# Kernel optimization log

Measured on AMD Instinct MI355X. Metric: run time of the kernel, lower is better.

The kernel has to match this reference:

```python
import jax, jax.numpy as jnp
import numpy as np

EMBED_DIM = 1024
NUM_HEADS = 16
HEAD_DIM = EMBED_DIM // NUM_HEADS
B, T = 2, 2048


def setup_inputs() -> dict:
    key = jax.random.key(0)
    ks = jax.random.split(key, 5)
    s_in = 1.0 / np.sqrt(EMBED_DIM)
    return {
        "x": jax.random.normal(ks[0], (B, T, EMBED_DIM), dtype=jnp.float32),
        "qkv_w": jax.random.uniform(ks[1], (3 * EMBED_DIM, EMBED_DIM), jnp.float32, -s_in, s_in),
        "qkv_b": jax.random.uniform(ks[2], (3 * EMBED_DIM,), jnp.float32, -s_in, s_in),
        "out_w": jax.random.uniform(ks[3], (EMBED_DIM, EMBED_DIM), jnp.float32, -s_in, s_in),
        "out_b": jax.random.uniform(ks[4], (EMBED_DIM,), jnp.float32, -s_in, s_in),
    }


def reference(x, qkv_w, qkv_b, out_w, out_b):
    b, t, d = x.shape
    scale = HEAD_DIM ** -0.5
    # fused qkv projection: (B, T, 3D)
    qkv = jnp.einsum("btd,ed->bte", x, qkv_w) + qkv_b
    qkv = qkv.reshape(b, t, 3, NUM_HEADS, HEAD_DIM)
    q, k, v = jnp.moveaxis(qkv, 2, 0)  # each (B, T, H, Dh)
    # scores: (B, H, T, T)
    scores = jnp.einsum("bqhd,bkhd->bhqk", q, k) * scale
    attn = jax.nn.softmax(scores, axis=-1)
    # attention output: (B, T, H, Dh) -> (B, T, D)
    ctx = jnp.einsum("bhqk,bkhd->bqhd", attn, v).reshape(b, t, d)
    return jnp.einsum("btd,ed->bte", ctx, out_w) + out_b
```

## Files before the change

kernel.cpp:

```cpp
#include <hip/hip_runtime.h>

typedef __bf16 bf16;
typedef __bf16 bf16x4 __attribute__((ext_vector_type(4)));
typedef __bf16 bf16x8 __attribute__((ext_vector_type(8)));
typedef _Float16 f16;
typedef _Float16 f16x4 __attribute__((ext_vector_type(4)));
typedef _Float16 f16x8 __attribute__((ext_vector_type(8)));
typedef float f32x4 __attribute__((ext_vector_type(4)));
typedef unsigned int uint2t __attribute__((ext_vector_type(2)));
typedef unsigned int uint4t __attribute__((ext_vector_type(4)));

#define MFMA16(a, b, c) __builtin_amdgcn_mfma_f32_16x16x32_bf16(a, b, c, 0, 0, 0)
#define MFMA16F(a, b, c) __builtin_amdgcn_mfma_f32_16x16x32_f16(a, b, c, 0, 0, 0)

__device__ __forceinline__ void lds_load16(void* lds, const void* g) {
  __builtin_amdgcn_global_load_lds(
      (const __attribute__((address_space(1))) unsigned int*)g,
      (__attribute__((address_space(3))) unsigned int*)lds, 16, 0, 0);
}

__global__ void cvt3(const float* __restrict__ x, const float* __restrict__ qw,
                     const float* __restrict__ ow, bf16* __restrict__ xb,
                     bf16* __restrict__ qwb, f16* __restrict__ owb) {
  const int i = blockIdx.x * blockDim.x + threadIdx.x;
  if (i < 1048576 + 786432) {
    const float* src;
    bf16* dst;
    int k;
    if (i < 1048576) {
      src = x; dst = xb; k = i;
    } else {
      src = qw; dst = qwb; k = i - 1048576;
    }
    const float4 v = ((const float4*)src)[k];
    bf16x4 o;
    o[0] = (bf16)v.x; o[1] = (bf16)v.y; o[2] = (bf16)v.z; o[3] = (bf16)v.w;
    ((bf16x4*)dst)[k] = o;
  } else {
    const int k = i - (1048576 + 786432);
    const float4 v = ((const float4*)ow)[k];
    f16x4 o;
    o[0] = (f16)v.x; o[1] = (f16)v.y; o[2] = (f16)v.z; o[3] = (f16)v.w;
    ((f16x4*)owb)[k] = o;
  }
}

__global__ __launch_bounds__(256, 2) void gemm_qkv(
    const bf16* __restrict__ A, const bf16* __restrict__ B,
    const float* __restrict__ bias, bf16* __restrict__ Qb,
    bf16* __restrict__ KF, f16* __restrict__ VF) {
  const int K = 1024;
  __shared__ bf16 As[128][64];
  __shared__ bf16 Bs[128][64];
  const int tid = threadIdx.x;
  const int w = tid >> 6, lane = tid & 63;
  const int l15 = lane & 15, quad = lane >> 4;
  const int lr = lane >> 3;
  const int lcs = ((lane & 7) ^ lr) * 8;
  const int sw = l15 & 7;
  const int blk = blockIdx.x;
  const int xslot = blk & 7, rest = blk >> 3;
  const int bm = xslot * 4 + (rest & 3);
  const int bn = rest >> 2;
  const int wm = (w >> 1) * 64, wn = (w & 1) * 64;

  const bf16* Abase = A + (size_t)(bm * 128) * K;
  const bf16* Bbase = B + (size_t)(bn * 128) * K;

  f32x4 acc[4][4] = {};

  for (int k0 = 0; k0 < K; k0 += 64) {
#pragma unroll
    for (int c = 0; c < 4; ++c) {
      const int row = w * 32 + c * 8;
      lds_load16(&As[row][0], Abase + (size_t)(row + lr) * K + k0 + lcs);
      lds_load16(&Bs[row][0], Bbase + (size_t)(row + lr) * K + k0 + lcs);
    }
    __syncthreads();
#pragma unroll
    for (int kk = 0; kk < 64; kk += 32) {
      const int cb = kk >> 3;
      bf16x8 am[4], bnf[4];
#pragma unroll
      for (int i = 0; i < 4; ++i)
        am[i] = *(const bf16x8*)&As[wm + i * 16 + l15][((cb + quad) ^ sw) * 8];
#pragma unroll
      for (int j = 0; j < 4; ++j)
        bnf[j] = *(const bf16x8*)&Bs[wn + j * 16 + l15][((cb + quad) ^ sw) * 8];
#pragma unroll
      for (int i = 0; i < 4; ++i)
#pragma unroll
        for (int j = 0; j < 4; ++j)
          acc[i][j] = MFMA16(am[i], bnf[j], acc[i][j]);
    }
    __syncthreads();
  }

#pragma unroll
  for (int j = 0; j < 4; ++j) {
    const int gcol = bn * 128 + wn + j * 16 + l15;
    const float bv = bias[gcol];
#pragma unroll
    for (int i = 0; i < 4; ++i) {
      const int t0 = bm * 128 + wm + i * 16 + quad * 4;
      if (gcol < 1024) {
#pragma unroll
        for (int r = 0; r < 4; ++r)
          Qb[(size_t)(t0 + r) * 1024 + gcol] =
              (bf16)((acc[i][j][r] + bv) * 0.18033688f);
      } else if (gcol < 2048) {
        const int dhl = gcol - 1024;
        const int hh = dhl >> 6, dh = dhl & 63;
        const int tl = t0 & 2047, bb = t0 >> 11;
        const size_t frag = ((size_t)(bb * 16 + hh) * 32 + (tl >> 6)) * 8 +
                            ((tl & 63) >> 4) * 2 + (dh >> 5);
        bf16* p = &KF[frag * 512 +
                      (size_t)(((dh >> 3) & 3) * 16 + (tl & 15)) * 8 + (dh & 7)];
#pragma unroll
        for (int r = 0; r < 4; ++r) p[r * 8] = (bf16)(acc[i][j][r] + bv);
      } else {
        const int dhl = gcol - 2048;
        const int hh = dhl >> 6, dh = dhl & 63;
        const int tl = t0 & 2047, bb = t0 >> 11;
        const size_t frag = ((size_t)(bb * 16 + hh) * 32 + (tl >> 6)) * 8 +
                            (dh >> 4) * 2 + ((tl & 63) >> 5);
        f16x4 pv;
#pragma unroll
        for (int r = 0; r < 4; ++r) pv[r] = (f16)(acc[i][j][r] + bv);
        *(f16x4*)&VF[frag * 512 +
                     (size_t)(((tl & 31) >> 3) * 16 + (dh & 15)) * 8 +
                     (tl & 7)] = pv;
      }
    }
  }
}

__global__ __launch_bounds__(256, 2) void gemm_out(
    const f16* __restrict__ A, const f16* __restrict__ B,
    const float* __restrict__ bias, float* __restrict__ Cf) {
  __shared__ f16 As[64][64];
  __shared__ f16 Bs[128][64];
  const int tid = threadIdx.x;
  const int w = tid >> 6, lane = tid & 63;
  const int l15 = lane & 15, quad = lane >> 4;
  const int lr = lane >> 3;
  const int lcs = ((lane & 7) ^ lr) * 8;
  const int sw = l15 & 7;
  const int blk = blockIdx.x;
  const int xslot = blk & 7, rest = blk >> 3;
  const int bm = xslot * 8 + (rest & 7);
  const int bn = rest >> 3;

  const f16* Abase = A + (size_t)(bm * 64) * 1024;
  const f16* Bbase = B + (size_t)(bn * 128) * 1024;

  f32x4 acc[4][2] = {};

  for (int k0 = 0; k0 < 1024; k0 += 64) {
#pragma unroll
    for (int c = 0; c < 2; ++c) {
      const int row = w * 16 + c * 8;
      lds_load16(&As[row][0], Abase + (size_t)(row + lr) * 1024 + k0 + lcs);
    }
#pragma unroll
    for (int c = 0; c < 4; ++c) {
      const int row = w * 32 + c * 8;
      lds_load16(&Bs[row][0], Bbase + (size_t)(row + lr) * 1024 + k0 + lcs);
    }
    __syncthreads();
#pragma unroll
    for (int kk = 0; kk < 64; kk += 32) {
      const int cb = kk >> 3;
      f16x8 am[4], bnf[2];
#pragma unroll
      for (int i = 0; i < 4; ++i)
        am[i] = *(const f16x8*)&As[i * 16 + l15][((cb + quad) ^ sw) * 8];
#pragma unroll
      for (int j = 0; j < 2; ++j)
        bnf[j] =
            *(const f16x8*)&Bs[w * 32 + j * 16 + l15][((cb + quad) ^ sw) * 8];
#pragma unroll
      for (int i = 0; i < 4; ++i)
#pragma unroll
        for (int j = 0; j < 2; ++j)
          acc[i][j] = MFMA16F(am[i], bnf[j], acc[i][j]);
    }
    __syncthreads();
  }

#pragma unroll
  for (int j = 0; j < 2; ++j) {
    const int gcol = bn * 128 + w * 32 + j * 16 + l15;
    const float bv = bias[gcol];
#pragma unroll
    for (int i = 0; i < 4; ++i)
#pragma unroll
      for (int r = 0; r < 4; ++r) {
        const int grow = bm * 64 + i * 16 + quad * 4 + r;
        Cf[(size_t)grow * 1024 + gcol] = acc[i][j][r] + bv;
      }
  }
}

__global__ __launch_bounds__(512, 4) void attn(const bf16* __restrict__ Qb,
                                               const bf16* __restrict__ KF,
                                               const f16* __restrict__ VF,
                                               f16* __restrict__ CTX) {
  __shared__ bf16 KV[2][2][2][4096];
  const int tid = threadIdx.x, w = tid >> 6, lane = tid & 63;
  const int g = w >> 2, wg = w & 3;
  const int l15 = lane & 15, quad = lane >> 4;
  const int blk = blockIdx.x;
  const int slot = blk & 7, grp = blk >> 3;
  const int qt = grp & 15, bh = (grp >> 4) * 8 + slot;
  const int h = bh & 15, b = bh >> 4;
  const int q0 = qt * 128;

  const bf16* qrow0 =
      Qb + (size_t)(b * 2048 + q0 + wg * 32 + l15) * 1024 + h * 64;
  const bf16* qrow1 = qrow0 + (size_t)16 * 1024;
  const bf16x8 bq0a = *(const bf16x8*)&qrow0[quad * 8];
  const bf16x8 bq0b = *(const bf16x8*)&qrow0[32 + quad * 8];
  const bf16x8 bq1a = *(const bf16x8*)&qrow1[quad * 8];
  const bf16x8 bq1b = *(const bf16x8*)&qrow1[32 + quad * 8];

  const bf16* kfs = KF + (size_t)(b * 16 + h) * 131072 + (size_t)g * 65536;
  const f16* vfs = VF + (size_t)(b * 16 + h) * 131072 + (size_t)g * 65536;
  const int so = wg * 1024;

#pragma unroll
  for (int c = 0; c < 2; ++c) {
    lds_load16(&KV[g][0][0][so + c * 512], kfs + so + c * 512 + lane * 8);
    lds_load16(&KV[g][1][0][so + c * 512], vfs + so + c * 512 + lane * 8);
  }

  const f16x8 ones8 = {(f16)1, (f16)1, (f16)1, (f16)1,
                       (f16)1, (f16)1, (f16)1, (f16)1};
  f32x4 lsum[2] = {};
  f32x4 o[2][4] = {};

  for (int kt = 0; kt < 16; ++kt) {
    const int cur = kt & 1;
    const bf16* kcur = &KV[g][0][cur][0];
    const f16* vcur = (const f16*)&KV[g][1][cur][0];
    __syncthreads();

    if (kt < 15) {
      const size_t nb = (size_t)(kt + 1) * 4096;
#pragma unroll
      for (int c = 0; c < 2; ++c) {
        lds_load16(&KV[g][0][cur ^ 1][so + c * 512],
                   kfs + nb + so + c * 512 + lane * 8);
        lds_load16(&KV[g][1][cur ^ 1][so + c * 512],
                   vfs + nb + so + c * 512 + lane * 8);
      }
    }

    f32x4 s[2][4] = {};
#pragma unroll
    for (int k2 = 0; k2 < 2; ++k2)
#pragma unroll
      for (int j = 0; j < 4; ++j) {
        const bf16x8 ak = *(const bf16x8*)&kcur[(j * 2 + k2) * 512 + lane * 8];
        s[0][j] = MFMA16(ak, k2 ? bq0b : bq0a, s[0][j]);
        s[1][j] = MFMA16(ak, k2 ? bq1b : bq1a, s[1][j]);
      }

    f16x8 bp[2][2];
#pragma unroll
    for (int i = 0; i < 2; ++i) {
      uint2t pd[4];
#pragma unroll
      for (int j = 0; j < 4; ++j) {
        const auto lo =
            __builtin_amdgcn_cvt_pkrtz(__builtin_amdgcn_exp2f(s[i][j][0]),
                                       __builtin_amdgcn_exp2f(s[i][j][1]));
        const auto hi =
            __builtin_amdgcn_cvt_pkrtz(__builtin_amdgcn_exp2f(s[i][j][2]),
                                       __builtin_amdgcn_exp2f(s[i][j][3]));
        pd[j][0] = __builtin_bit_cast(unsigned, lo);
        pd[j][1] = __builtin_bit_cast(unsigned, hi);
      }
#pragma unroll
      for (int k2 = 0; k2 < 2; ++k2) {
        uint4t wd;
#pragma unroll
        for (int d = 0; d < 2; ++d) {
          unsigned pa = pd[2 * k2][d], pb = pd[2 * k2 + 1][d];
          asm("v_permlane32_swap_b32 %0, %1" : "+v"(pa), "+v"(pb));
          asm("v_permlane16_swap_b32 %0, %1" : "+v"(pa), "+v"(pb));
          wd[d] = pa;
          wd[2 + d] = pb;
        }
        bp[i][k2] = __builtin_bit_cast(f16x8, wd);
      }
    }

#pragma unroll
    for (int k2 = 0; k2 < 2; ++k2) {
#pragma unroll
      for (int j = 0; j < 4; ++j) {
        const f16x8 av = *(const f16x8*)&vcur[(j * 2 + k2) * 512 + lane * 8];
        o[0][j] = MFMA16F(av, bp[0][k2], o[0][j]);
        o[1][j] = MFMA16F(av, bp[1][k2], o[1][j]);
      }
      lsum[0] = MFMA16F(ones8, bp[0][k2], lsum[0]);
      lsum[1] = MFMA16F(ones8, bp[1][k2], lsum[1]);
    }
  }

  __syncthreads();
  float* ob = (float*)&KV[0][0][0][0];
  float* lb = ob + 128 * 68;
  if (g == 1) {
#pragma unroll
    for (int i = 0; i < 2; ++i) {
      const int q = wg * 32 + i * 16 + l15;
#pragma unroll
      for (int j = 0; j < 4; ++j)
        *(f32x4*)&ob[q * 68 + j * 16 + quad * 4] = o[i][j];
      if (quad == 0) lb[q] = lsum[i][0];
    }
  }
  __syncthreads();
  if (g == 0) {
#pragma unroll
    for (int i = 0; i < 2; ++i) {
      const int q = wg * 32 + i * 16 + l15;
      const float inv = 1.f / (lsum[i][0] + lb[q]);
      f16* crow = CTX + (size_t)(b * 2048 + q0 + q) * 1024 + h * 64;
#pragma unroll
      for (int j = 0; j < 4; ++j) {
        const f32x4 ox = o[i][j] + *(const f32x4*)&ob[q * 68 + j * 16 + quad * 4];
        f16x4 ov;
#pragma unroll
        for (int r = 0; r < 4; ++r) ov[r] = (f16)(ox[r] * inv);
        *(f16x4*)&crow[j * 16 + quad * 4] = ov;
      }
    }
  }
}

extern "C" void kernel_launch(void* const* d_in, const int* in_sizes, int n_in,
                              void* d_out, int out_size, void* d_ws,
                              size_t ws_size, hipStream_t stream) {
  const float* x = (const float*)d_in[0];
  const float* qkv_w = (const float*)d_in[1];
  const float* qkv_b = (const float*)d_in[2];
  const float* out_w = (const float*)d_in[3];
  const float* out_b = (const float*)d_in[4];
  float* out = (float*)d_out;

  bf16* base = (bf16*)d_ws;
  bf16* xb = base;
  bf16* wqkv = base + (size_t)4096 * 1024;
  f16* wout = (f16*)(base + (size_t)7168 * 1024);
  bf16* qb = base + (size_t)8192 * 1024;
  bf16* kf = base + (size_t)12288 * 1024;
  f16* vf = (f16*)(base + (size_t)16384 * 1024);
  f16* ctx = (f16*)(base + (size_t)20480 * 1024);

  cvt3<<<2097152 / 256, 256, 0, stream>>>(x, qkv_w, out_w, xb, wqkv, wout);

  gemm_qkv<<<768, 256, 0, stream>>>(xb, wqkv, qkv_b, qb, kf, vf);
  attn<<<512, 512, 0, stream>>>(qb, kf, vf, ctx);
  gemm_out<<<512, 256, 0, stream>>>(ctx, wout, out_b, out);
}
```

Before: 169.4 us.

## Restructure attention blocks: drop key-split, one 16-row tile per wave

The attention kernel previously split the key range across two wave groups of 4 waves each, with each wave covering 32 query rows, and merged partial outputs through LDS at the end. Now each 256-thread block handles 64 queries, with each wave covering 16 rows and iterating over all 32 key tiles. The kernel launches twice as many blocks. This removes the cross-group reduction, its barriers and the per-block LDS footprint. In exchange, each block streams twice as many K/V tiles sequentially, and K/V reuse per LDS load is halved, so global and LDS traffic goes up.

```diff
diff --git a/kernel.cpp b/kernel.cpp
--- a/kernel.cpp
+++ b/kernel.cpp
@@ -202,98 +202,90 @@
   }
 }
 
-__global__ __launch_bounds__(512, 4) void attn(const bf16* __restrict__ Qb,
+__global__ __launch_bounds__(256, 4) void attn(const bf16* __restrict__ Qb,
                                                const bf16* __restrict__ KF,
                                                const f16* __restrict__ VF,
                                                f16* __restrict__ CTX) {
-  __shared__ bf16 KV[2][2][2][4096];
+  __shared__ bf16 KV[2][2][4096];
   const int tid = threadIdx.x, w = tid >> 6, lane = tid & 63;
-  const int g = w >> 2, wg = w & 3;
   const int l15 = lane & 15, quad = lane >> 4;
   const int blk = blockIdx.x;
   const int slot = blk & 7, grp = blk >> 3;
-  const int qt = grp & 15, bh = (grp >> 4) * 8 + slot;
+  const int qt = grp & 31, bh = (grp >> 5) * 8 + slot;
   const int h = bh & 15, b = bh >> 4;
-  const int q0 = qt * 128;
-
-  const bf16* qrow0 =
-      Qb + (size_t)(b * 2048 + q0 + wg * 32 + l15) * 1024 + h * 64;
-  const bf16* qrow1 = qrow0 + (size_t)16 * 1024;
-  const bf16x8 bq0a = *(const bf16x8*)&qrow0[quad * 8];
-  const bf16x8 bq0b = *(const bf16x8*)&qrow0[32 + quad * 8];
-  const bf16x8 bq1a = *(const bf16x8*)&qrow1[quad * 8];
-  const bf16x8 bq1b = *(const bf16x8*)&qrow1[32 + quad * 8];
-
-  const bf16* kfs = KF + (size_t)(b * 16 + h) * 131072 + (size_t)g * 65536;
-  const f16* vfs = VF + (size_t)(b * 16 + h) * 131072 + (size_t)g * 65536;
-  const int so = wg * 1024;
+  const int q0 = qt * 64;
+
+  const bf16* qrow =
+      Qb + (size_t)(b * 2048 + q0 + w * 16 + l15) * 1024 + h * 64;
+  const bf16x8 bqa = *(const bf16x8*)&qrow[quad * 8];
+  const bf16x8 bqb = *(const bf16x8*)&qrow[32 + quad * 8];
+
+  const bf16* kfs = KF + (size_t)(b * 16 + h) * 131072;
+  const f16* vfs = VF + (size_t)(b * 16 + h) * 131072;
+  const int so = w * 1024;
 
 #pragma unroll
   for (int c = 0; c < 2; ++c) {
-    lds_load16(&KV[g][0][0][so + c * 512], kfs + so + c * 512 + lane * 8);
-    lds_load16(&KV[g][1][0][so + c * 512], vfs + so + c * 512 + lane * 8);
+    lds_load16(&KV[0][0][so + c * 512], kfs + so + c * 512 + lane * 8);
+    lds_load16(&KV[1][0][so + c * 512], vfs + so + c * 512 + lane * 8);
   }
 
   const f16x8 ones8 = {(f16)1, (f16)1, (f16)1, (f16)1,
                        (f16)1, (f16)1, (f16)1, (f16)1};
-  f32x4 lsum[2] = {};
-  f32x4 o[2][4] = {};
-
-  for (int kt = 0; kt < 16; ++kt) {
+  f32x4 lsum = {};
+  f32x4 o[4] = {};
+
+  for (int kt = 0; kt < 32; ++kt) {
     const int cur = kt & 1;
-    const bf16* kcur = &KV[g][0][cur][0];
-    const f16* vcur = (const f16*)&KV[g][1][cur][0];
-    __syncthreads();
-
-    if (kt < 15) {
+    const bf16* kcur = &KV[0][cur][0];
+    const f16* vcur = (const f16*)&KV[1][cur][0];
+    __syncthreads();
+
+    if (kt < 31) {
       const size_t nb = (size_t)(kt + 1) * 4096;
 #pragma unroll
       for (int c = 0; c < 2; ++c) {
-        lds_load16(&KV[g][0][cur ^ 1][so + c * 512],
+        lds_load16(&KV[0][cur ^ 1][so + c * 512],
                    kfs + nb + so + c * 512 + lane * 8);
-        lds_load16(&KV[g][1][cur ^ 1][so + c * 512],
+        lds_load16(&KV[1][cur ^ 1][so + c * 512],
                    vfs + nb + so + c * 512 + lane * 8);
       }
     }
 
-    f32x4 s[2][4] = {};
+    f32x4 s[4] = {};
 #pragma unroll
     for (int k2 = 0; k2 < 2; ++k2)
 #pragma unroll
       for (int j = 0; j < 4; ++j) {
         const bf16x8 ak = *(const bf16x8*)&kcur[(j * 2 + k2) * 512 + lane * 8];
-        s[0][j] = MFMA16(ak, k2 ? bq0b : bq0a, s[0][j]);
-        s[1][j] = MFMA16(ak, k2 ? bq1b : bq1a, s[1][j]);
-      }
-
-    f16x8 bp[2][2];
-#pragma unroll
-    for (int i = 0; i < 2; ++i) {
-      uint2t pd[4];
-#pragma unroll
-      for (int j = 0; j < 4; ++j) {
-        const auto lo =
-            __builtin_amdgcn_cvt_pkrtz(__builtin_amdgcn_exp2f(s[i][j][0]),
-                                       __builtin_amdgcn_exp2f(s[i][j][1]));
-        const auto hi =
-            __builtin_amdgcn_cvt_pkrtz(__builtin_amdgcn_exp2f(s[i][j][2]),
-                                       __builtin_amdgcn_exp2f(s[i][j][3]));
-        pd[j][0] = __builtin_bit_cast(unsigned, lo);
-        pd[j][1] = __builtin_bit_cast(unsigned, hi);
-      }
-#pragma unroll
-      for (int k2 = 0; k2 < 2; ++k2) {
-        uint4t wd;
-#pragma unroll
-        for (int d = 0; d < 2; ++d) {
-          unsigned pa = pd[2 * k2][d], pb = pd[2 * k2 + 1][d];
-          asm("v_permlane32_swap_b32 %0, %1" : "+v"(pa), "+v"(pb));
-          asm("v_permlane16_swap_b32 %0, %1" : "+v"(pa), "+v"(pb));
-          wd[d] = pa;
-          wd[2 + d] = pb;
-        }
-        bp[i][k2] = __builtin_bit_cast(f16x8, wd);
-      }
+        s[j] = MFMA16(ak, k2 ? bqb : bqa, s[j]);
+      }
+
+    uint2t pd[4];
+#pragma unroll
+    for (int j = 0; j < 4; ++j) {
+      const auto lo =
+          __builtin_amdgcn_cvt_pkrtz(__builtin_amdgcn_exp2f(s[j][0]),
+                                     __builtin_amdgcn_exp2f(s[j][1]));
+      const auto hi =
+          __builtin_amdgcn_cvt_pkrtz(__builtin_amdgcn_exp2f(s[j][2]),
+                                     __builtin_amdgcn_exp2f(s[j][3]));
+      pd[j][0] = __builtin_bit_cast(unsigned, lo);
+      pd[j][1] = __builtin_bit_cast(unsigned, hi);
+    }
+    f16x8 bp[2];
+#pragma unroll
+    for (int k2 = 0; k2 < 2; ++k2) {
+      uint4t wd;
+#pragma unroll
+      for (int d = 0; d < 2; ++d) {
+        unsigned pa = pd[2 * k2][d], pb = pd[2 * k2 + 1][d];
+        asm("v_permlane32_swap_b32 %0, %1" : "+v"(pa), "+v"(pb));
+        asm("v_permlane16_swap_b32 %0, %1" : "+v"(pa), "+v"(pb));
+        wd[d] = pa;
+        wd[2 + d] = pb;
+      }
+      bp[k2] = __builtin_bit_cast(f16x8, wd);
     }
 
 #pragma unroll
@@ -301,43 +293,20 @@
 #pragma unroll
       for (int j = 0; j < 4; ++j) {
         const f16x8 av = *(const f16x8*)&vcur[(j * 2 + k2) * 512 + lane * 8];
-        o[0][j] = MFMA16F(av, bp[0][k2], o[0][j]);
-        o[1][j] = MFMA16F(av, bp[1][k2], o[1][j]);
-      }
-      lsum[0] = MFMA16F(ones8, bp[0][k2], lsum[0]);
-      lsum[1] = MFMA16F(ones8, bp[1][k2], lsum[1]);
-    }
-  }
-
-  __syncthreads();
-  float* ob = (float*)&KV[0][0][0][0];
-  float* lb = ob + 128 * 68;
-  if (g == 1) {
-#pragma unroll
-    for (int i = 0; i < 2; ++i) {
-      const int q = wg * 32 + i * 16 + l15;
-#pragma unroll
-      for (int j = 0; j < 4; ++j)
-        *(f32x4*)&ob[q * 68 + j * 16 + quad * 4] = o[i][j];
-      if (quad == 0) lb[q] = lsum[i][0];
-    }
-  }
-  __syncthreads();
-  if (g == 0) {
-#pragma unroll
-    for (int i = 0; i < 2; ++i) {
-      const int q = wg * 32 + i * 16 + l15;
-      const float inv = 1.f / (lsum[i][0] + lb[q]);
-      f16* crow = CTX + (size_t)(b * 2048 + q0 + q) * 1024 + h * 64;
-#pragma unroll
-      for (int j = 0; j < 4; ++j) {
-        const f32x4 ox = o[i][j] + *(const f32x4*)&ob[q * 68 + j * 16 + quad * 4];
-        f16x4 ov;
-#pragma unroll
-        for (int r = 0; r < 4; ++r) ov[r] = (f16)(ox[r] * inv);
-        *(f16x4*)&crow[j * 16 + quad * 4] = ov;
-      }
-    }
+        o[j] = MFMA16F(av, bp[k2], o[j]);
+      }
+      lsum = MFMA16F(ones8, bp[k2], lsum);
+    }
+  }
+
+  const float inv = 1.f / lsum[0];
+  f16* crow = CTX + (size_t)(b * 2048 + q0 + w * 16 + l15) * 1024 + h * 64;
+#pragma unroll
+  for (int j = 0; j < 4; ++j) {
+    f16x4 ov;
+#pragma unroll
+    for (int r = 0; r < 4; ++r) ov[r] = (f16)(o[j][r] * inv);
+    *(f16x4*)&crow[j * 16 + quad * 4] = ov;
   }
 }
 
@@ -363,6 +332,6 @@
   cvt3<<<2097152 / 256, 256, 0, stream>>>(x, qkv_w, out_w, xb, wqkv, wout);
 
   gemm_qkv<<<768, 256, 0, stream>>>(xb, wqkv, qkv_b, qb, kf, vf);
-  attn<<<512, 512, 0, stream>>>(qb, kf, vf, ctx);
+  attn<<<1024, 256, 0, stream>>>(qb, kf, vf, ctx);
   gemm_out<<<512, 256, 0, stream>>>(ctx, wout, out_b, out);
 }
```

Result: slower. 174.7 us (+3.2%).
